# Kernel optimization log

Hardware: AMD Instinct MI355X
Metric: run time of the kernel (lower is better)

Reference implementation:

```python
import jax, jax.numpy as jnp
import numpy as np

M = 4096
N = 4096


def precompute_expk(n):
    # Twiddle factors exp(-i*pi*k/(2n)), k = 0..n-1 (matches DREAMPlace precompute_expk)
    k = jnp.arange(n)
    return jnp.exp(-1j * jnp.pi * k.astype(jnp.float32) / (2.0 * n)).astype(jnp.complex64)


def setup_inputs() -> dict:
    key = jax.random.key(0)
    x = jax.random.normal(key, (M, N), dtype=jnp.float32)
    return {"x": x, "expkM": precompute_expk(M), "expkN": precompute_expk(N)}


def _dct1d(x, expk):
    """DCT-II along the last axis via Makhoul's even/odd reorder + FFT + twiddle.

    y[k] = sum_n x[n] * cos(pi * (2n+1) * k / (2L))  (unnormalized, no factor 2)
    """
    # reorder: even-indexed samples forward, odd-indexed samples reversed
    v = jnp.concatenate([x[..., 0::2], x[..., 1::2][..., ::-1]], axis=-1)
    V = jnp.fft.fft(v, axis=-1)
    return jnp.real(V * expk)


def reference(x, expkM, expkN):
    # 2D DCT-II: transform columns (length N), then rows (length M)
    y = _dct1d(x, expkN)            # [M, N], DCT along axis -1
    y = _dct1d(y.T, expkM).T        # DCT along axis 0
    return y
```

## Files before the change

kernel.cpp:

```cpp
#include <hip/hip_runtime.h>
#include <hip/hip_bf16.h>


#define L 4096

__device__ __forceinline__ int SWZ(int e) {
    return e ^ (((e >> 4) ^ (e >> 8)) & 15);
}

__device__ __forceinline__ float2 cmul(float2 a, float2 b) {
    return make_float2(a.x * b.x - a.y * b.y, a.x * b.y + a.y * b.x);
}

__device__ __forceinline__ void bfly4(float2& x0, float2& x1, float2& x2, float2& x3) {
    float t0x = x0.x + x2.x, t0y = x0.y + x2.y;
    float t1x = x0.x - x2.x, t1y = x0.y - x2.y;
    float t2x = x1.x + x3.x, t2y = x1.y + x3.y;
    float t3x = x1.x - x3.x, t3y = x1.y - x3.y;
    x0 = make_float2(t0x + t2x, t0y + t2y);
    x1 = make_float2(t1x + t3y, t1y - t3x);
    x2 = make_float2(t0x - t2x, t0y - t2y);
    x3 = make_float2(t1x - t3y, t1y + t3x);
}

template <int M>
__device__ __forceinline__ float2 W64T() {
    constexpr float C[17] = {1.f, 0.995184726672197f, 0.980785280403230f,
        0.956940335732209f, 0.923879532511287f, 0.881921264348355f,
        0.831469612302545f, 0.773010453362737f, 0.707106781186548f,
        0.634393284163645f, 0.555570233019602f, 0.471396736825998f,
        0.382683432365090f, 0.290284677254462f, 0.195090322016128f,
        0.098017140329561f, 0.f};
    constexpr int m = M & 63;
    constexpr float c = (m <= 16) ?  C[m]
                      : (m <= 32) ? -C[32 - m]
                      : (m <= 48) ? -C[m - 32]
                      :              C[64 - m];
    constexpr float s = (m <= 16) ?  C[16 - m]
                      : (m <= 32) ?  C[m - 16]
                      : (m <= 48) ? -C[48 - m]
                      :             -C[m - 48];
    return make_float2(c, -s);
}

#define FOR8(X) X(0) X(1) X(2) X(3) X(4) X(5) X(6) X(7)

#define FFT8N(P) \
  bfly4(P##0, P##2, P##4, P##6); \
  bfly4(P##1, P##3, P##5, P##7); \
  { float2 e1_=P##2, e2_=P##4, e3_=P##6, o0_=P##1, o1_=P##3, o2_=P##5, o3_=P##7; \
    o1_ = cmul(o1_, make_float2(0.70710678118654752f, -0.70710678118654752f)); \
    o2_ = make_float2(o2_.y, -o2_.x); \
    o3_ = cmul(o3_, make_float2(-0.70710678118654752f, -0.70710678118654752f)); \
    float2 e0_=P##0; \
    P##0 = make_float2(e0_.x+o0_.x, e0_.y+o0_.y); \
    P##4 = make_float2(e0_.x-o0_.x, e0_.y-o0_.y); \
    P##1 = make_float2(e1_.x+o1_.x, e1_.y+o1_.y); \
    P##5 = make_float2(e1_.x-o1_.x, e1_.y-o1_.y); \
    P##2 = make_float2(e2_.x+o2_.x, e2_.y+o2_.y); \
    P##6 = make_float2(e2_.x-o2_.x, e2_.y-o2_.y); \
    P##3 = make_float2(e3_.x+o3_.x, e3_.y+o3_.y); \
    P##7 = make_float2(e3_.x-o3_.x, e3_.y-o3_.y); }


template <int Q>
__device__ __forceinline__ void stage_pair(float2* lds, int t) {
    const int j = t & (Q - 1);
    const int G = t / Q;
    const int base = G * 16 * Q + j;

    float2 v[4][4];
#pragma unroll
    for (int b = 0; b < 4; ++b)
#pragma unroll
        for (int a = 0; a < 4; ++a)
            v[a][b] = lds[SWZ(base + (a + 4 * b) * Q)];

    if (Q > 1) {
        float c1, s1;
        __sincosf((float)j * (-6.2831853071795864769f / (4.0f * (float)Q)), &s1, &c1);
        float2 w1 = make_float2(c1, s1);
        float2 w2 = cmul(w1, w1);
        float2 w3 = cmul(w2, w1);
#pragma unroll
        for (int b = 0; b < 4; ++b) {
            v[1][b] = cmul(v[1][b], w1);
            v[2][b] = cmul(v[2][b], w2);
            v[3][b] = cmul(v[3][b], w3);
        }
    }
#pragma unroll
    for (int b = 0; b < 4; ++b) bfly4(v[0][b], v[1][b], v[2][b], v[3][b]);

    float2 u;
    if (Q == 1) {
        u = make_float2(1.0f, 0.0f);
    } else {
        float cu, su;
        __sincosf((float)j * (-6.2831853071795864769f / (16.0f * (float)Q)), &su, &cu);
        u = make_float2(cu, su);
    }
    const float2 E = make_float2(0.92387953251128674f, -0.38268343236508977f);
    float2 w = u;
#pragma unroll
    for (int a = 0; a < 4; ++a) {
        if (!(Q == 1 && a == 0)) {
            float2 W2 = cmul(w, w);
            float2 W3 = cmul(W2, w);
            v[a][1] = cmul(v[a][1], w);
            v[a][2] = cmul(v[a][2], W2);
            v[a][3] = cmul(v[a][3], W3);
        }
        bfly4(v[a][0], v[a][1], v[a][2], v[a][3]);
        if (a < 3) w = cmul(w, E);
    }

#pragma unroll
    for (int b = 0; b < 4; ++b)
#pragma unroll
        for (int a = 0; a < 4; ++a)
            lds[SWZ(base + (a + 4 * b) * Q)] = v[a][b];
}

__global__ __launch_bounds__(256)
void dct_rows2_kernel(const float* __restrict__ in, float* __restrict__ out) {
    __shared__ float2 lds[L];

    const int r0 = blockIdx.x * 2;
    const int t = threadIdx.x;
    const float* rowA = in + (size_t)r0 * L;
    const float* rowB = rowA + L;

    const int revT4 = ((t & 3) << 6) | ((t & 12) << 2) | ((t >> 2) & 12) | ((t >> 6) & 3);

#pragma unroll
    for (int w = 0; w < 8; ++w) {
        int n = w * 256 + t;
        float2 fa = *reinterpret_cast<const float2*>(&rowA[2 * n]);
        float2 fb = *reinterpret_cast<const float2*>(&rowB[2 * n]);
        int p = (revT4 << 4) | ((w & 3) << 2) | (w >> 2);
        lds[SWZ(p)]        = make_float2(fa.x, fb.x);
        lds[SWZ(4095 - p)] = make_float2(fa.y, fb.y);
    }
    __syncthreads();

    stage_pair<1>(lds, t);
    __syncthreads();
    stage_pair<16>(lds, t);
    __syncthreads();
    stage_pair<256>(lds, t);
    __syncthreads();

    float* outA = out + (size_t)r0 * L;
    float* outB = outA + L;

    float2 e;
    __sincosf((float)t * 3.8349519697141029e-4f, &e.y, &e.x);
    const float2 ST = make_float2(0.99518472667219693f, 0.09801714032956060f);
#pragma unroll
    for (int w = 0; w < 16; ++w) {
        int k = w * 256 + t;
        float2 Zk = lds[SWZ(k)];
        int m = (L - k) & (L - 1);
        float2 Zm = lds[SWZ(m)];

        float vax = 0.5f * (Zk.x + Zm.x);
        float vay = 0.5f * (Zk.y - Zm.y);
        float vbx = 0.5f * (Zk.y + Zm.y);
        float vby = 0.5f * (Zm.x - Zk.x);

        outA[k] = vax * e.x + vay * e.y;
        outB[k] = vbx * e.x + vby * e.y;
        e = cmul(e, ST);
    }
}

__global__ __launch_bounds__(512)
void fft64_col_a2(const float* __restrict__ Y, float* __restrict__ ws) {
    __shared__ float2 xch[4096];
    const int c = threadIdx.x & 63;
    const int v = threadIdx.x >> 6;
    const int b = blockIdx.x;
    const int T = blockIdx.y;
    const int ca = T * 128 + c;
    const int cb = ca + 64;

#define LDA(u) float2 g##u; { \
        const int aa = 8 * u + v; \
        const int row = (u < 4) ? (128 * aa + 2 * b) : (8191 - 128 * aa - 2 * b); \
        const float* rp = Y + (size_t)row * L; \
        g##u = make_float2(rp[ca], rp[cb]); }
    FOR8(LDA)
#undef LDA

    FFT8N(g)

#define WRA(t) xch[v * 512 + t * 64 + c] = g##t;
    FOR8(WRA)
#undef WRA
    __syncthreads();
#define RDA(vv) g##vv = xch[vv * 512 + v * 64 + c];
    FOR8(RDA)
#undef RDA

    float2 wv; __sincosf((float)v * -0.09817477042468103f, &wv.y, &wv.x);
    {
        float2 f = wv;
        g1 = cmul(g1, f); f = cmul(f, wv);
        g2 = cmul(g2, f); f = cmul(f, wv);
        g3 = cmul(g3, f); f = cmul(f, wv);
        g4 = cmul(g4, f); f = cmul(f, wv);
        g5 = cmul(g5, f); f = cmul(f, wv);
        g6 = cmul(g6, f); f = cmul(f, wv);
        g7 = cmul(g7, f);
    }

    FFT8N(g)

    float2 mw, ms;
    __sincosf((float)(b * v) * -1.5339807878856412e-3f, &mw.y, &mw.x);
    __sincosf((float)b * -1.2271846303085130e-2f, &ms.y, &ms.x);
    float2* wp = reinterpret_cast<float2*>(ws) + (size_t)b * 2048 + (size_t)T * 64 + c;
#define STA(s) { \
        g##s = cmul(g##s, mw); \
        wp[(size_t)(8 * s + v) * 131072] = g##s; \
        mw = cmul(mw, ms); }
    FOR8(STA)
#undef STA
}

__global__ __launch_bounds__(512)
void fft64_col_b2(const float* __restrict__ wsf, float* __restrict__ out) {
    __shared__ float2 xch[8192];
    const int c  = threadIdx.x & 63;
    const int v  = threadIdx.x >> 6;
    const int qa = blockIdx.x;
    const int T  = blockIdx.y;
    const int q  = qa;
    const int q2 = (qa == 0) ? 32 : 64 - qa;
    const bool self0 = (qa == 0);

    const float2* wsc = reinterpret_cast<const float2*>(wsf);
    const size_t cbase = (size_t)T * 64 + c;

#define LDH(u) \
    float2 ha##u = wsc[(size_t)q  * 131072 + (size_t)(8*u+v) * 2048 + cbase]; \
    float2 hp##u = wsc[(size_t)q2 * 131072 + (size_t)(8*u+v) * 2048 + cbase];
    FOR8(LDH)
#undef LDH

    float2 wv; __sincosf((float)v * -0.09817477042468103f, &wv.y, &wv.x);
#define MKF(u) float2 fc##u = cmul(W64T<8*u>(), wv);
    FOR8(MKF)
#undef MKF

    const float2 STEP = make_float2(0.98078528040323045f, 0.19509032201612827f);

    for (int r = 0; r < 4; ++r) {
        const int qr  = (r < 2) ? q : q2;
        const int isB = r & 1;
        const bool sw = (r >= 2);
        const int buf = (r & 1) * 4096;

#define MKSEQ(u) float2 g##u; { \
        float2 hh = sw ? hp##u : ha##u; \
        float2 pp = self0 ? hh : (sw ? ha##u : hp##u); \
        float2 cj = make_float2(pp.x, -pp.y); \
        float2 mm = (qr == 0) ? cj : cmul(cj, fc##u); \
        if (!isB) g##u = make_float2(0.5f * (hh.x + mm.x), 0.5f * (hh.y + mm.y)); \
        else      g##u = make_float2(0.5f * (hh.y - mm.y), -0.5f * (hh.x - mm.x)); }
        FOR8(MKSEQ)
#undef MKSEQ

        FFT8N(g)

#define WRX(k) xch[buf + v * 512 + k * 64 + c] = g##k;
        FOR8(WRX)
#undef WRX
        __syncthreads();
#define RDX(vv) g##vv = xch[buf + vv * 512 + v * 64 + c];
        FOR8(RDX)
#undef RDX

        {
            float2 f = wv;
            g1 = cmul(g1, f); f = cmul(f, wv);
            g2 = cmul(g2, f); f = cmul(f, wv);
            g3 = cmul(g3, f); f = cmul(f, wv);
            g4 = cmul(g4, f); f = cmul(f, wv);
            g5 = cmul(g5, f); f = cmul(f, wv);
            g6 = cmul(g6, f); f = cmul(f, wv);
            g7 = cmul(g7, f);
        }

        FFT8N(g)

        float2 e; __sincosf((float)(64 * v + qr) * 3.8349519697141029e-4f, &e.y, &e.x);
        const int colb = T * 128 + c + (isB ? 64 : 0);
#define EP(a2) { \
        out[(size_t)(512 * a2 + 64 * v + qr) * L + colb] = g##a2.x * e.x + g##a2.y * e.y; \
        e = cmul(e, STEP); }
        FOR8(EP)
#undef EP
    }
}

extern "C" void kernel_launch(void* const* d_in, const int* in_sizes, int n_in,
                              void* d_out, int out_size, void* d_ws, size_t ws_size,
                              hipStream_t stream) {
    const float* x = (const float*)d_in[0];
    float* out = (float*)d_out;
    float* ws  = (float*)d_ws;

    dct_rows2_kernel<<<L / 2, 256, 0, stream>>>(x, out);
    fft64_col_a2<<<dim3(64, 32), 512, 0, stream>>>(out, ws);
    fft64_col_b2<<<dim3(32, 32), 512, 0, stream>>>(ws, out);
}
```

Measured before the change: 88.12 us.

## Run two 64-point FFTs then split spectra instead of four pre-twiddled FFTs

The column second-stage kernel used to build four separated sequences (A/B for q and q2) in the frequency domain and run four 64-point FFTs per block. It now runs only two FFTs, on the packed q and q2 inputs, stores both results in shared memory, and separates the two real-signal spectra afterwards through a conjugate-mirror combine before the twiddle epilogue. This halves the FFT arithmetic and LDS exchange rounds, at the cost of extra shared-memory reads with reversed indexing and additional barriers.

```diff
diff --git a/kernel.cpp b/kernel.cpp
--- a/kernel.cpp
+++ b/kernel.cpp
@@ -21,26 +21,6 @@
     x1 = make_float2(t1x + t3y, t1y - t3x);
     x2 = make_float2(t0x - t2x, t0y - t2y);
     x3 = make_float2(t1x - t3y, t1y + t3x);
-}
-
-template <int M>
-__device__ __forceinline__ float2 W64T() {
-    constexpr float C[17] = {1.f, 0.995184726672197f, 0.980785280403230f,
-        0.956940335732209f, 0.923879532511287f, 0.881921264348355f,
-        0.831469612302545f, 0.773010453362737f, 0.707106781186548f,
-        0.634393284163645f, 0.555570233019602f, 0.471396736825998f,
-        0.382683432365090f, 0.290284677254462f, 0.195090322016128f,
-        0.098017140329561f, 0.f};
-    constexpr int m = M & 63;
-    constexpr float c = (m <= 16) ?  C[m]
-                      : (m <= 32) ? -C[32 - m]
-                      : (m <= 48) ? -C[m - 32]
-                      :              C[64 - m];
-    constexpr float s = (m <= 16) ?  C[16 - m]
-                      : (m <= 32) ?  C[m - 16]
-                      : (m <= 48) ? -C[48 - m]
-                      :             -C[m - 48];
-    return make_float2(c, -s);
 }
 
 #define FOR8(X) X(0) X(1) X(2) X(3) X(4) X(5) X(6) X(7)
@@ -62,6 +42,15 @@
     P##3 = make_float2(e3_.x+o3_.x, e3_.y+o3_.y); \
     P##7 = make_float2(e3_.x-o3_.x, e3_.y-o3_.y); }
 
+#define TWCHAIN(P, W) { float2 f_ = W; \
+    P##1 = cmul(P##1, f_); f_ = cmul(f_, W); \
+    P##2 = cmul(P##2, f_); f_ = cmul(f_, W); \
+    P##3 = cmul(P##3, f_); f_ = cmul(f_, W); \
+    P##4 = cmul(P##4, f_); f_ = cmul(f_, W); \
+    P##5 = cmul(P##5, f_); f_ = cmul(f_, W); \
+    P##6 = cmul(P##6, f_); f_ = cmul(f_, W); \
+    P##7 = cmul(P##7, f_); }
+
 
 template <int Q>
 __device__ __forceinline__ void stage_pair(float2* lds, int t) {
@@ -204,16 +193,7 @@
 #undef RDA
 
     float2 wv; __sincosf((float)v * -0.09817477042468103f, &wv.y, &wv.x);
-    {
-        float2 f = wv;
-        g1 = cmul(g1, f); f = cmul(f, wv);
-        g2 = cmul(g2, f); f = cmul(f, wv);
-        g3 = cmul(g3, f); f = cmul(f, wv);
-        g4 = cmul(g4, f); f = cmul(f, wv);
-        g5 = cmul(g5, f); f = cmul(f, wv);
-        g6 = cmul(g6, f); f = cmul(f, wv);
-        g7 = cmul(g7, f);
-    }
+    TWCHAIN(g, wv)
 
     FFT8N(g)
 
@@ -230,7 +210,7 @@
 }
 
 __global__ __launch_bounds__(512)
-void fft64_col_b2(const float* __restrict__ wsf, float* __restrict__ out) {
+void fft64_col_b3(const float* __restrict__ wsf, float* __restrict__ out) {
     __shared__ float2 xch[8192];
     const int c  = threadIdx.x & 63;
     const int v  = threadIdx.x >> 6;
@@ -238,7 +218,6 @@
     const int T  = blockIdx.y;
     const int q  = qa;
     const int q2 = (qa == 0) ? 32 : 64 - qa;
-    const bool self0 = (qa == 0);
 
     const float2* wsc = reinterpret_cast<const float2*>(wsf);
     const size_t cbase = (size_t)T * 64 + c;
@@ -250,59 +229,67 @@
 #undef LDH
 
     float2 wv; __sincosf((float)v * -0.09817477042468103f, &wv.y, &wv.x);
-#define MKF(u) float2 fc##u = cmul(W64T<8*u>(), wv);
-    FOR8(MKF)
-#undef MKF
+
+    FFT8N(ha)
+#define W1(k) xch[v * 512 + k * 64 + c] = ha##k;
+    FOR8(W1)
+#undef W1
+    __syncthreads();
+#define DECLG(i) float2 g##i;
+    FOR8(DECLG)
+#undef DECLG
+#define R1(vv) g##vv = xch[vv * 512 + v * 64 + c];
+    FOR8(R1)
+#undef R1
+    TWCHAIN(g, wv)
+    FFT8N(g)
+
+#define SV(a) float2 gq##a = g##a; xch[4096 + (8*a + v) * 64 + c] = g##a;
+    FOR8(SV)
+#undef SV
+    __syncthreads();
+
+    FFT8N(hp)
+#define W2(k) xch[v * 512 + k * 64 + c] = hp##k;
+    FOR8(W2)
+#undef W2
+    __syncthreads();
+#define R2(vv) g##vv = xch[vv * 512 + v * 64 + c];
+    FOR8(R2)
+#undef R2
+    TWCHAIN(g, wv)
+    FFT8N(g)
+    __syncthreads();
+#define W3(a) xch[(8*a + v) * 64 + c] = g##a;
+    FOR8(W3)
+#undef W3
+    __syncthreads();
 
     const float2 STEP = make_float2(0.98078528040323045f, 0.19509032201612827f);
-
-    for (int r = 0; r < 4; ++r) {
-        const int qr  = (r < 2) ? q : q2;
-        const int isB = r & 1;
-        const bool sw = (r >= 2);
-        const int buf = (r & 1) * 4096;
-
-#define MKSEQ(u) float2 g##u; { \
-        float2 hh = sw ? hp##u : ha##u; \
-        float2 pp = self0 ? hh : (sw ? ha##u : hp##u); \
-        float2 cj = make_float2(pp.x, -pp.y); \
-        float2 mm = (qr == 0) ? cj : cmul(cj, fc##u); \
-        if (!isB) g##u = make_float2(0.5f * (hh.x + mm.x), 0.5f * (hh.y + mm.y)); \
-        else      g##u = make_float2(0.5f * (hh.y - mm.y), -0.5f * (hh.x - mm.x)); }
-        FOR8(MKSEQ)
-#undef MKSEQ
-
-        FFT8N(g)
-
-#define WRX(k) xch[buf + v * 512 + k * 64 + c] = g##k;
-        FOR8(WRX)
-#undef WRX
-        __syncthreads();
-#define RDX(vv) g##vv = xch[buf + vv * 512 + v * 64 + c];
-        FOR8(RDX)
-#undef RDX
-
-        {
-            float2 f = wv;
-            g1 = cmul(g1, f); f = cmul(f, wv);
-            g2 = cmul(g2, f); f = cmul(f, wv);
-            g3 = cmul(g3, f); f = cmul(f, wv);
-            g4 = cmul(g4, f); f = cmul(f, wv);
-            g5 = cmul(g5, f); f = cmul(f, wv);
-            g6 = cmul(g6, f); f = cmul(f, wv);
-            g7 = cmul(g7, f);
-        }
-
-        FFT8N(g)
-
-        float2 e; __sincosf((float)(64 * v + qr) * 3.8349519697141029e-4f, &e.y, &e.x);
-        const int colb = T * 128 + c + (isB ? 64 : 0);
-#define EP(a2) { \
-        out[(size_t)(512 * a2 + 64 * v + qr) * L + colb] = g##a2.x * e.x + g##a2.y * e.y; \
-        e = cmul(e, STEP); }
-        FOR8(EP)
-#undef EP
-    }
+    float2 eq, eq2;
+    __sincosf((float)(64 * v + q ) * 3.8349519697141029e-4f, &eq.y,  &eq.x);
+    __sincosf((float)(64 * v + q2) * 3.8349519697141029e-4f, &eq2.y, &eq2.x);
+    const int colA = T * 128 + c;
+
+#define CMB(a) { \
+    const int p_ = 8 * a + v; \
+    float2 rq  = (qa == 0) ? xch[4096 + (((64 - p_) & 63) * 64) + c] \
+                           : xch[(63 - p_) * 64 + c]; \
+    float2 rq2 = (qa == 0) ? xch[(63 - p_) * 64 + c] \
+                           : xch[4096 + (63 - p_) * 64 + c]; \
+    float FAx = 0.5f * (gq##a.x + rq.x), FAy = 0.5f * (gq##a.y - rq.y); \
+    float FBx = 0.5f * (gq##a.y + rq.y), FBy = 0.5f * (rq.x - gq##a.x); \
+    size_t rowq = (size_t)(512 * a + 64 * v + q) * L; \
+    out[rowq + colA]      = FAx * eq.x + FAy * eq.y; \
+    out[rowq + colA + 64] = FBx * eq.x + FBy * eq.y; \
+    float GAx = 0.5f * (g##a.x + rq2.x), GAy = 0.5f * (g##a.y - rq2.y); \
+    float GBx = 0.5f * (g##a.y + rq2.y), GBy = 0.5f * (rq2.x - g##a.x); \
+    size_t rowq2 = (size_t)(512 * a + 64 * v + q2) * L; \
+    out[rowq2 + colA]      = GAx * eq2.x + GAy * eq2.y; \
+    out[rowq2 + colA + 64] = GBx * eq2.x + GBy * eq2.y; \
+    eq = cmul(eq, STEP); eq2 = cmul(eq2, STEP); }
+    FOR8(CMB)
+#undef CMB
 }
 
 extern "C" void kernel_launch(void* const* d_in, const int* in_sizes, int n_in,
@@ -314,5 +301,5 @@
 
     dct_rows2_kernel<<<L / 2, 256, 0, stream>>>(x, out);
     fft64_col_a2<<<dim3(64, 32), 512, 0, stream>>>(out, ws);
-    fft64_col_b2<<<dim3(32, 32), 512, 0, stream>>>(ws, out);
-}
+    fft64_col_b3<<<dim3(32, 32), 512, 0, stream>>>(ws, out);
+}
```

Measured after the change: 79.95 us. 1.1x faster.
